# Kernel tuning notes

Measured on AMD Instinct MI355X. Metric: run time of the kernel, lower is better.

## Reference

```python
import jax, jax.numpy as jnp
import numpy as np
import math

HIDDEN = 2048
HEADS = 16
R = HIDDEN // HEADS  # 128
B, S = 4, 2048


def setup_inputs() -> dict:
    key = jax.random.key(0)
    ks = jax.random.split(key, 11)
    sc_h = 1.0 / math.sqrt(HIDDEN)
    return {
        "q": jax.random.normal(ks[0], (B, S, HIDDEN), jnp.float32),
        "k": jax.random.normal(ks[1], (B, S, HIDDEN), jnp.float32),
        "v": jax.random.normal(ks[2], (B, S, HIDDEN), jnp.float32),
        # Linear params, stored as [in, out] so y = x @ W + b
        "wqs_w": jax.random.normal(ks[3], (HIDDEN, HEADS), jnp.float32) * sc_h,
        "wqs_b": jnp.zeros((HEADS,), jnp.float32),
        "wks_w": jax.random.normal(ks[4], (HIDDEN, HEADS), jnp.float32) * sc_h,
        "wks_b": jnp.zeros((HEADS,), jnp.float32),
        "wvs_w": jax.random.normal(ks[5], (HIDDEN, HIDDEN), jnp.float32) * sc_h,
        "wvs_b": jnp.zeros((HIDDEN,), jnp.float32),
        "wo_w": jax.random.normal(ks[6], (HIDDEN, HIDDEN), jnp.float32) * sc_h,
        "wo_b": jnp.zeros((HIDDEN,), jnp.float32),
    }


def reference(q, k, v, wqs_w, wqs_b, wks_w, wks_b, wvs_w, wvs_b, wo_w, wo_b):
    # Low-rank QK: Q, K are [B, S, HEADS] (tiny score space), V is [B, S, HIDDEN].
    # NOTE: faithful to source, V is projected from k (v arg is unused).
    Q = q @ wqs_w + wqs_b                      # [B, S, HEADS]
    K = k @ wks_w + wks_b                      # [B, S, HEADS]
    V = k @ wvs_w + wvs_b                      # [B, S, HIDDEN]
    scale = 1.0 / math.sqrt(R)
    logits = jnp.einsum("bqh,bkh->bqk", Q, K) * scale   # [B, S, S]
    score = jax.nn.softmax(logits, axis=-1)
    values = jnp.einsum("bqk,bkd->bqd", score, V)       # [B, S, HIDDEN]
    # reshape(batch, -1, attn_heads*r) is a no-op here.
    out = values @ wo_w + wo_b                 # dropout in eval mode -> identity
    return out
```

## Files before the change

### kernel.cpp

```cpp
#include <hip/hip_runtime.h>
#include <hip/hip_bf16.h>

#define NB 4
#define SEQ 2048
#define HID 2048

typedef short bf16x8 __attribute__((ext_vector_type(8)));
typedef float f32x4 __attribute__((ext_vector_type(4)));

__device__ __forceinline__ unsigned short f2b(float f) {
  union { float f; unsigned int u; } v; v.f = f;
  unsigned int r = v.u + 0x7fffu + ((v.u >> 16) & 1u);
  return (unsigned short)(r >> 16);
}
__device__ __forceinline__ float blo(unsigned int u) {
  union { unsigned int u; float f; } t; t.u = u << 16; return t.f;
}
__device__ __forceinline__ float bhi(unsigned int u) {
  union { unsigned int u; float f; } t; t.u = u & 0xffff0000u; return t.f;
}

__device__ __forceinline__ void gload_lds16(const unsigned short* g, unsigned short* l) {
  __builtin_amdgcn_global_load_lds(
      (const __attribute__((address_space(1))) unsigned int*)g,
      (__attribute__((address_space(3))) unsigned int*)l, 16, 0, 0);
}

__global__ __launch_bounds__(256) void convert_bf16(const float* __restrict__ X,
                                                    unsigned short* __restrict__ Y, int n8) {
  int stride = gridDim.x * 256;
  for (int i = blockIdx.x * 256 + threadIdx.x; i < n8; i += stride) {
    long o = (long)i * 8;
    float4 a = *(const float4*)(X + o);
    float4 b = *(const float4*)(X + o + 4);
    uint4 p;
    p.x = (unsigned)f2b(a.x) | ((unsigned)f2b(a.y) << 16);
    p.y = (unsigned)f2b(a.z) | ((unsigned)f2b(a.w) << 16);
    p.z = (unsigned)f2b(b.x) | ((unsigned)f2b(b.y) << 16);
    p.w = (unsigned)f2b(b.z) | ((unsigned)f2b(b.w) << 16);
    *(uint4*)(Y + o) = p;
  }
}

__global__ __launch_bounds__(256) void transpose_conv(const float* __restrict__ X,
                                                      unsigned short* __restrict__ Y,
                                                      int R, int C) {
  __shared__ float T[64][65];
  int r0 = blockIdx.y * 64, c0 = blockIdx.x * 64;
  int tx = threadIdx.x & 63, ty = threadIdx.x >> 6;
#pragma unroll
  for (int i = 0; i < 16; ++i) {
    int r = ty + i * 4;
    T[r][tx] = X[(long)(r0 + r) * C + c0 + tx];
  }
  __syncthreads();
#pragma unroll
  for (int i = 0; i < 16; ++i) {
    int c = ty + i * 4;
    Y[(long)(c0 + c) * R + r0 + tx] = f2b(T[tx][c]);
  }
}

__global__ __launch_bounds__(256) void wt_prep(const float* __restrict__ W,
                                               unsigned short* __restrict__ WT) {
  __shared__ float T[16][17];
  int t = threadIdx.x;
  int k0 = blockIdx.x * 16;
  T[t >> 4][t & 15] = W[k0 * 16 + t];
  __syncthreads();
  int h = t >> 4, kk = t & 15;
  WT[h * 2048 + k0 + kk] = f2b(T[kk][h]);
}

__global__ void bias_init(const float* __restrict__ wo_b, float* __restrict__ c) {
  int j = blockIdx.x * 256 + threadIdx.x;
  c[j] = wo_b[j];
}
__global__ void bias_accum(const float* __restrict__ wvs_b, const float* __restrict__ wo_w,
                           float* __restrict__ c) {
  int j = blockIdx.x * 256 + threadIdx.x;
  int t0 = blockIdx.y * 128;
  float p = 0.f;
  for (int t = 0; t < 128; ++t) p += wvs_b[t0 + t] * wo_w[(long)(t0 + t) * HID + j];
  atomicAdd(&c[j], p);
}

__global__ __launch_bounds__(256) void proj_mfma(
    const float* __restrict__ Xq, const float* __restrict__ Xk,
    const unsigned short* __restrict__ WTq, const unsigned short* __restrict__ WTk,
    const float* __restrict__ bq, const float* __restrict__ bk,
    float* __restrict__ Yq, float* __restrict__ Yk,
    unsigned short* __restrict__ kbf) {
  __shared__ unsigned short Xs[64 * 256];
  const int tid = threadIdx.x;
  const int lane = tid & 63, wave = tid >> 6;
  const bool isK = (blockIdx.y == 1);
  const float* X = isK ? Xk : Xq;
  const unsigned short* WT = isK ? WTk : WTq;
  const float* bias = isK ? bk : bq;
  float* Y = isK ? Yk : Yq;
  const long row0 = (long)blockIdx.x * 64;
  const float* Xb = X + row0 * HID;

  f32x4 acc = {0.f, 0.f, 0.f, 0.f};
  float4 regs[16];
#pragma unroll
  for (int i = 0; i < 16; ++i)
    regs[i] = *(const float4*)(Xb + (long)(i * 4 + wave) * HID + lane * 4);

  const int arow = wave * 16 + (lane & 15);
  const int rowb = arow * 512;
  const int swzA = (arow & 7) << 4;
  const int g16 = (lane >> 4) * 16;

  for (int c = 0; c < 8; ++c) {
    ushort4 cv[16];
#pragma unroll
    for (int i = 0; i < 16; ++i) {
      cv[i].x = f2b(regs[i].x); cv[i].y = f2b(regs[i].y);
      cv[i].z = f2b(regs[i].z); cv[i].w = f2b(regs[i].w);
    }
#pragma unroll
    for (int i = 0; i < 16; ++i) {
      int r = i * 4 + wave;
      int b = r * 512 + ((lane * 8) ^ ((r & 7) << 4));
      *(ushort4*)((char*)Xs + b) = cv[i];
    }
    if (isK) {
#pragma unroll
      for (int i = 0; i < 16; ++i)
        *(ushort4*)(kbf + (row0 + i * 4 + wave) * (long)HID + c * 256 + lane * 4) = cv[i];
    }
    __syncthreads();
    if (c < 7) {
#pragma unroll
      for (int i = 0; i < 16; ++i)
        regs[i] = *(const float4*)(Xb + (long)(i * 4 + wave) * HID + (c + 1) * 256 + lane * 4);
    }
    const unsigned short* WTc = WT + (lane & 15) * 2048 + c * 256 + (lane >> 4) * 8;
#pragma unroll
    for (int kk = 0; kk < 8; ++kk) {
      int b = rowb + ((kk * 64 + g16) ^ swzA);
      bf16x8 af = *(const bf16x8*)((const char*)Xs + b);
      bf16x8 wf = *(const bf16x8*)(WTc + kk * 32);
      acc = __builtin_amdgcn_mfma_f32_16x16x32_bf16(af, wf, acc, 0, 0, 0);
    }
    __syncthreads();
  }
  const int ci = lane & 15;
  const int rg = (lane >> 4) * 4;
  float bb = bias[ci];
#pragma unroll
  for (int i = 0; i < 4; ++i) {
    long r = row0 + wave * 16 + rg + i;
    Y[r * 16 + ci] = acc[i] + bb;
  }
}

__global__ __launch_bounds__(256) void attn_softmax(const float* __restrict__ Qf,
                                                    const float* __restrict__ Kf,
                                                    unsigned short* __restrict__ P) {
  __shared__ unsigned short Kl[SEQ * 16];
  int b = blockIdx.y;
  const float* Kb = Kf + (long)b * SEQ * 16;
  int tid = threadIdx.x;
  for (int i = tid * 8; i < SEQ * 16; i += 256 * 8) {
    float4 a = *(const float4*)(Kb + i);
    float4 b4 = *(const float4*)(Kb + i + 4);
    uint4 p;
    p.x = (unsigned)f2b(a.x) | ((unsigned)f2b(a.y) << 16);
    p.y = (unsigned)f2b(a.z) | ((unsigned)f2b(a.w) << 16);
    p.z = (unsigned)f2b(b4.x) | ((unsigned)f2b(b4.y) << 16);
    p.w = (unsigned)f2b(b4.z) | ((unsigned)f2b(b4.w) << 16);
    *(uint4*)&Kl[i] = p;
  }
  __syncthreads();
  int lane = tid & 63, wave = tid >> 6;
  int q0 = blockIdx.x * 32 + wave * 8;
  const float scale = 0.08838834764831845f;
  for (int r = q0; r < q0 + 8; ++r) {
    const float* qp = Qf + ((long)b * SEQ + r) * 16;
    float qv[16];
#pragma unroll
    for (int h = 0; h < 16; h += 4) {
      float4 t = *(const float4*)(qp + h);
      qv[h] = t.x; qv[h + 1] = t.y; qv[h + 2] = t.z; qv[h + 3] = t.w;
    }
    float pv[32];
    float mx = -1e30f;
#pragma unroll
    for (int c = 0; c < 32; ++c) {
      const uint4* kp = (const uint4*)&Kl[(c * 64 + lane) * 16];
      uint4 k0 = kp[0], k1 = kp[1];
      float a = 0.f;
      a += qv[0]  * blo(k0.x) + qv[1]  * bhi(k0.x);
      a += qv[2]  * blo(k0.y) + qv[3]  * bhi(k0.y);
      a += qv[4]  * blo(k0.z) + qv[5]  * bhi(k0.z);
      a += qv[6]  * blo(k0.w) + qv[7]  * bhi(k0.w);
      a += qv[8]  * blo(k1.x) + qv[9]  * bhi(k1.x);
      a += qv[10] * blo(k1.y) + qv[11] * bhi(k1.y);
      a += qv[12] * blo(k1.z) + qv[13] * bhi(k1.z);
      a += qv[14] * blo(k1.w) + qv[15] * bhi(k1.w);
      pv[c] = a * scale;
      mx = fmaxf(mx, pv[c]);
    }
#pragma unroll
    for (int m = 1; m < 64; m <<= 1) mx = fmaxf(mx, __shfl_xor(mx, m, 64));
    float sum = 0.f;
#pragma unroll
    for (int c = 0; c < 32; ++c) { pv[c] = __expf(pv[c] - mx); sum += pv[c]; }
#pragma unroll
    for (int m = 1; m < 64; m <<= 1) sum += __shfl_xor(sum, m, 64);
    float inv = 1.f / sum;
    unsigned short* Pr = P + ((long)b * SEQ + r) * SEQ;
#pragma unroll
    for (int c = 0; c < 32; ++c) Pr[c * 64 + lane] = f2b(pv[c] * inv);
  }
}

template <int MODE>
__global__ __launch_bounds__(256, 2) void gemm_bt(const unsigned short* __restrict__ A,
                                                  const unsigned short* __restrict__ Bt,
                                                  void* __restrict__ Cv,
                                                  const float* __restrict__ bias,
                                                  int K, long sA, long sB, long sC, int ldc) {
  __shared__ unsigned short As[128 * 64];
  __shared__ unsigned short Bs[128 * 64];
  const int tid = threadIdx.x;
  const int lane = tid & 63, wave = tid >> 6;
  A += blockIdx.z * sA;
  Bt += blockIdx.z * sB;
  const long bm = (long)blockIdx.y * 128, bn = (long)blockIdx.x * 128;
  const int wm = (wave >> 1) * 64, wn = (wave & 1) * 64;
  f32x4 acc[4][4] = {};
  const unsigned short* gA = A + (bm + wave * 32 + (lane >> 3)) * (long)K + (lane & 7) * 8;
  const unsigned short* gB = Bt + (bn + wave * 32 + (lane >> 3)) * (long)K + (lane & 7) * 8;
  unsigned short* lA = &As[wave * 2048];
  unsigned short* lB = &Bs[wave * 2048];
  const int nkt = K >> 6;
  for (int kt = 0; kt < nkt; ++kt) {
    const unsigned short* ga = gA + kt * 64;
    const unsigned short* gb = gB + kt * 64;
#pragma unroll
    for (int c = 0; c < 4; ++c) {
      gload_lds16(ga + (long)c * 8 * K, lA + c * 512);
      gload_lds16(gb + (long)c * 8 * K, lB + c * 512);
    }
    __syncthreads();
#pragma unroll
    for (int ks = 0; ks < 2; ++ks) {
      bf16x8 af[4], bfr[4];
#pragma unroll
      for (int m = 0; m < 4; ++m)
        af[m] = *(const bf16x8*)&As[(wm + m * 16 + (lane & 15)) * 64 + ks * 32 + (lane >> 4) * 8];
#pragma unroll
      for (int n = 0; n < 4; ++n)
        bfr[n] = *(const bf16x8*)&Bs[(wn + n * 16 + (lane & 15)) * 64 + ks * 32 + (lane >> 4) * 8];
#pragma unroll
      for (int m = 0; m < 4; ++m)
#pragma unroll
        for (int n = 0; n < 4; ++n)
          acc[m][n] = __builtin_amdgcn_mfma_f32_16x16x32_bf16(af[m], bfr[n], acc[m][n], 0, 0, 0);
    }
    __syncthreads();
  }
  const int rg = (lane >> 4) * 4;
  const int ci = lane & 15;
#pragma unroll
  for (int m = 0; m < 4; ++m) {
#pragma unroll
    for (int n = 0; n < 4; ++n) {
      long gr0 = bm + wm + m * 16 + rg;
      long gc = bn + wn + n * 16 + ci;
      if (MODE == 0) {
        unsigned short* C = (unsigned short*)Cv;
#pragma unroll
        for (int i = 0; i < 4; ++i) C[(gr0 + i) * (long)ldc + gc] = f2b(acc[m][n][i]);
      } else if (MODE == 1) {
        unsigned short* C = (unsigned short*)Cv;
        long addr = (gr0 >> 11) * (long)(SEQ * HID) + gc * SEQ + (gr0 & 2047);
        ushort4 v;
        v.x = f2b(acc[m][n][0]); v.y = f2b(acc[m][n][1]);
        v.z = f2b(acc[m][n][2]); v.w = f2b(acc[m][n][3]);
        *(ushort4*)(C + addr) = v;
      } else {
        float* C = (float*)Cv + (long)blockIdx.z * sC;
        float bb = bias[gc];
#pragma unroll
        for (int i = 0; i < 4; ++i) C[(gr0 + i) * (long)ldc + gc] = acc[m][n][i] + bb;
      }
    }
  }
}

extern "C" void kernel_launch(void* const* d_in, const int* in_sizes, int n_in,
                              void* d_out, int out_size, void* d_ws, size_t ws_size,
                              hipStream_t stream) {
  (void)in_sizes; (void)n_in; (void)out_size; (void)ws_size;
  const float* q     = (const float*)d_in[0];
  const float* k     = (const float*)d_in[1];
  const float* wqs_w = (const float*)d_in[3];
  const float* wqs_b = (const float*)d_in[4];
  const float* wks_w = (const float*)d_in[5];
  const float* wks_b = (const float*)d_in[6];
  const float* wvs_w = (const float*)d_in[7];
  const float* wvs_b = (const float*)d_in[8];
  const float* wo_w  = (const float*)d_in[9];
  const float* wo_b  = (const float*)d_in[10];

  char* ws = (char*)d_ws;
  const long MB = 1048576;
  const long KB = 1024;
  float* Qf            = (float*)(ws);
  float* Kf            = (float*)(ws + 512 * KB);
  float* cvec          = (float*)(ws + MB);
  unsigned short* WTq  = (unsigned short*)(ws + MB + 64 * KB);
  unsigned short* WTk  = (unsigned short*)(ws + MB + 128 * KB);
  unsigned short* kbf  = (unsigned short*)(ws + 2 * MB);
  unsigned short* P    = kbf;
  unsigned short* VwT  = (unsigned short*)(ws + 34 * MB);
  unsigned short* wvsbf= VwT;
  unsigned short* woT  = (unsigned short*)(ws + 42 * MB);
  unsigned short* W2T  = (unsigned short*)(ws + 66 * MB);

  wt_prep<<<128, 256, 0, stream>>>(wqs_w, WTq);
  wt_prep<<<128, 256, 0, stream>>>(wks_w, WTk);
  proj_mfma<<<dim3(128, 2), 256, 0, stream>>>(q, k, WTq, WTk, wqs_b, wks_b, Qf, Kf, kbf);
  convert_bf16<<<2048, 256, 0, stream>>>(wvs_w, wvsbf, (HID * HID) / 8);
  transpose_conv<<<dim3(32, 32), 256, 0, stream>>>(wo_w, woT, HID, HID);
  bias_init<<<8, 256, 0, stream>>>(wo_b, cvec);
  bias_accum<<<dim3(8, 16), 256, 0, stream>>>(wvs_b, wo_w, cvec);
  gemm_bt<0><<<dim3(16, 16, 1), 256, 0, stream>>>(woT, wvsbf, W2T, nullptr, HID, 0, 0, 0, HID);
  gemm_bt<1><<<dim3(16, 64, 1), 256, 0, stream>>>(kbf, W2T, VwT, nullptr, HID, 0, 0, 0, 0);
  attn_softmax<<<dim3(64, NB), 256, 0, stream>>>(Qf, Kf, P);
  gemm_bt<2><<<dim3(16, 16, NB), 256, 0, stream>>>(P, VwT, d_out, cvec, SEQ,
                                                   (long)SEQ * SEQ, (long)SEQ * HID,
                                                   (long)SEQ * HID, HID);
}
```

Baseline: 538.2 us.

## Add 256x256-tile double-buffered GEMM kernel for the two large matmuls

Adds a new 512-thread GEMM kernel with 256x256 output tiles, an XOR-swizzled LDS layout, double-buffered global-to-LDS loads, and a split of each K-step so the next stage is prefetched between two MFMA halves, with raised wave priority during the second half. The k·W2 projection and the P·V GEMM now use it instead of the 128-tile kernel. Larger tiles raise arithmetic intensity and cut global and LDS traffic per FLOP, and the split aims to overlap loads with compute. In exchange the kernel uses 128KB of LDS and many accumulator registers, which limits occupancy, and the P·V launch has only 256 blocks, which may underfill the GPU.

```diff
diff --git a/kernel.cpp b/kernel.cpp
--- a/kernel.cpp
+++ b/kernel.cpp
@@ -276,7 +276,110 @@
         unsigned short* C = (unsigned short*)Cv;
 #pragma unroll
         for (int i = 0; i < 4; ++i) C[(gr0 + i) * (long)ldc + gc] = f2b(acc[m][n][i]);
-      } else if (MODE == 1) {
+      } else {
+        float* C = (float*)Cv + (long)blockIdx.z * sC;
+        float bb = bias[gc];
+#pragma unroll
+        for (int i = 0; i < 4; ++i) C[(gr0 + i) * (long)ldc + gc] = acc[m][n][i] + bb;
+      }
+    }
+  }
+}
+
+template <int MODE>
+__global__ __launch_bounds__(512, 2) void gemm256(const unsigned short* __restrict__ A,
+                                                  const unsigned short* __restrict__ Bt,
+                                                  void* __restrict__ Cv,
+                                                  const float* __restrict__ bias,
+                                                  int K, long sA, long sB, long sC, int ldc) {
+  __shared__ unsigned short As[2][16384];
+  __shared__ unsigned short Bs[2][16384];
+  const int tid = threadIdx.x;
+  const int lane = tid & 63, wave = tid >> 6;
+  A += blockIdx.z * sA;
+  Bt += blockIdx.z * sB;
+  const long bm = (long)blockIdx.y * 256, bn = (long)blockIdx.x * 256;
+  const int wrow = (wave >> 2) * 128;
+  const int wcol = (wave & 3) * 64;
+
+  const int srow = tid >> 3;
+  const int scol8 = ((tid & 7) ^ (srow & 7)) * 8;
+  const unsigned short* gA = A + (bm + srow) * (long)K + scol8;
+  const unsigned short* gB = Bt + (bn + srow) * (long)K + scol8;
+  const int ldst = tid * 8;
+
+  const int swz = (lane & 7) << 4;
+  const int koff = (lane >> 4) * 16;
+  const int arow_b = (wrow + (lane & 15)) * 128;
+  const int brow_b = (wcol + (lane & 15)) * 128;
+
+  f32x4 acc[8][4] = {};
+  const int nt = K >> 6;
+
+#define STAGE256(kt, buf)                                                          \
+  {                                                                                \
+    _Pragma("unroll") for (int j = 0; j < 4; ++j) {                                \
+      gload_lds16(gA + (long)j * 64 * K + (kt) * 64, &As[buf][j * 4096 + ldst]);   \
+      gload_lds16(gB + (long)j * 64 * K + (kt) * 64, &Bs[buf][j * 4096 + ldst]);   \
+    }                                                                              \
+  }
+
+  STAGE256(0, 0);
+  STAGE256(1, 1);
+  asm volatile("s_waitcnt vmcnt(8)" ::: "memory");
+  __builtin_amdgcn_s_barrier();
+
+  int c = 0;
+  for (int t = 0; t < nt; ++t) {
+    const char* pa = (const char*)As[c];
+    const char* pb = (const char*)Bs[c];
+    bf16x8 a0[8], a1[8], b0[4], b1[4];
+#pragma unroll
+    for (int m = 0; m < 8; ++m) {
+      int rb = arow_b + m * 2048;
+      a0[m] = *(const bf16x8*)(pa + rb + ((koff) ^ swz));
+      a1[m] = *(const bf16x8*)(pa + rb + ((64 + koff) ^ swz));
+    }
+#pragma unroll
+    for (int n = 0; n < 4; ++n) {
+      int rb = brow_b + n * 2048;
+      b0[n] = *(const bf16x8*)(pb + rb + ((koff) ^ swz));
+      b1[n] = *(const bf16x8*)(pb + rb + ((64 + koff) ^ swz));
+    }
+#pragma unroll
+    for (int m = 0; m < 8; ++m)
+#pragma unroll
+      for (int n = 0; n < 4; ++n)
+        acc[m][n] = __builtin_amdgcn_mfma_f32_16x16x32_bf16(a0[m], b0[n], acc[m][n], 0, 0, 0);
+    asm volatile("s_waitcnt lgkmcnt(0)" ::: "memory");
+    __builtin_amdgcn_s_barrier();
+    if (t + 2 < nt) STAGE256(t + 2, c);
+    __builtin_amdgcn_s_setprio(1);
+#pragma unroll
+    for (int m = 0; m < 8; ++m)
+#pragma unroll
+      for (int n = 0; n < 4; ++n)
+        acc[m][n] = __builtin_amdgcn_mfma_f32_16x16x32_bf16(a1[m], b1[n], acc[m][n], 0, 0, 0);
+    __builtin_amdgcn_s_setprio(0);
+    if (t + 2 < nt) {
+      asm volatile("s_waitcnt vmcnt(8)" ::: "memory");
+    } else {
+      asm volatile("s_waitcnt vmcnt(0)" ::: "memory");
+    }
+    __builtin_amdgcn_s_barrier();
+    c ^= 1;
+  }
+#undef STAGE256
+
+  const int rg = (lane >> 4) * 4;
+  const int ci = lane & 15;
+#pragma unroll
+  for (int m = 0; m < 8; ++m) {
+#pragma unroll
+    for (int n = 0; n < 4; ++n) {
+      long gr0 = bm + wrow + m * 16 + rg;
+      long gc = bn + wcol + n * 16 + ci;
+      if (MODE == 1) {
         unsigned short* C = (unsigned short*)Cv;
         long addr = (gr0 >> 11) * (long)(SEQ * HID) + gc * SEQ + (gr0 & 2047);
         ushort4 v;
@@ -331,9 +434,9 @@
   bias_init<<<8, 256, 0, stream>>>(wo_b, cvec);
   bias_accum<<<dim3(8, 16), 256, 0, stream>>>(wvs_b, wo_w, cvec);
   gemm_bt<0><<<dim3(16, 16, 1), 256, 0, stream>>>(woT, wvsbf, W2T, nullptr, HID, 0, 0, 0, HID);
-  gemm_bt<1><<<dim3(16, 64, 1), 256, 0, stream>>>(kbf, W2T, VwT, nullptr, HID, 0, 0, 0, 0);
+  gemm256<1><<<dim3(8, 32, 1), 512, 0, stream>>>(kbf, W2T, VwT, nullptr, HID, 0, 0, 0, 0);
   attn_softmax<<<dim3(64, NB), 256, 0, stream>>>(Qf, Kf, P);
-  gemm_bt<2><<<dim3(16, 16, NB), 256, 0, stream>>>(P, VwT, d_out, cvec, SEQ,
-                                                   (long)SEQ * SEQ, (long)SEQ * HID,
-                                                   (long)SEQ * HID, HID);
-}
+  gemm256<2><<<dim3(8, 8, NB), 512, 0, stream>>>(P, VwT, d_out, cvec, SEQ,
+                                                 (long)SEQ * SEQ, (long)SEQ * HID,
+                                                 (long)SEQ * HID, HID);
+}
```

After: 494.7 us. 1.09x faster.
